# Performance work log

Hardware: AMD Instinct MI355X
Metric: run time of the kernel (lower is better)

## Reference

```python
import jax, jax.numpy as jnp
import numpy as np
from jax import lax

N_C = 1024  # number of FPS centroids (hard-coded in forward)
K = 32      # knn neighbors (hard-coded in forward)


def _fps(x, far0):
    # Faithful to the source: dist is recomputed against ONLY the latest
    # centroid each iteration (the mask/min-update in the source is dead code),
    # then far = argmax(dist).
    B = x.shape[0]
    bidx = jnp.arange(B)

    def step(far, _):
        c = x[bidx, far]                              # [B, C]
        d = jnp.sum((x - c[:, None, :]) ** 2, -1)     # [B, N]
        return jnp.argmax(d, -1), c

    _, cents = lax.scan(step, far0, None, length=N_C)  # cents: [n_c, B, C]
    return jnp.transpose(cents, (1, 0, 2))             # [B, n_c, C]


def _knn_group(x, cent):
    # squared euclidean distances (same argsort order as torch.cdist)
    d2 = (jnp.sum(cent ** 2, -1)[..., None]
          + jnp.sum(x ** 2, -1)[:, None, :]
          - 2.0 * jnp.einsum('bmc,bnc->bmn', cent, x))   # [B, n_c, N]
    _, idx = lax.top_k(-d2, K)                            # [B, n_c, K] smallest dists
    neighbors = jax.vmap(lambda xb, ib: xb[ib])(x, idx)   # [B, n_c, K, C]
    return neighbors


def _conv1x1(h, w, b):
    # 1x1 Conv1d == channel matmul; h: [B, Cin, L], w: [Cout, Cin]
    return jax.nn.relu(jnp.einsum('oi,bil->bol', w, h) + b[None, :, None])


def setup_inputs() -> dict:
    key = jax.random.key(0)
    ks = jax.random.split(key, 20)
    B, N, C = 4, 16384, 3
    num_classes = 3
    p = lambda k, shp: (jax.random.normal(k, shp, jnp.float32) * 0.02)
    return {
        'x': jax.random.normal(ks[0], (B, N, C), jnp.float32),
        'far_init': jax.random.randint(ks[1], (B,), 0, N, jnp.int32),
        'w1': p(ks[2], (64, 3)),    'b1': p(ks[3], (64,)),
        'w2': p(ks[4], (64, 64)),   'b2': p(ks[5], (64,)),
        'w3': p(ks[6], (64, 64)),   'b3': p(ks[7], (64,)),
        'w4': p(ks[8], (128, 64)),  'b4': p(ks[9], (128,)),
        'w5': p(ks[10], (1024, 128)), 'b5': p(ks[11], (1024,)),
        'fw1': p(ks[12], (512, 1024)), 'fb1': p(ks[13], (512,)),
        'fw2': p(ks[14], (256, 512)),  'fb2': p(ks[15], (256,)),
        'fw3': p(ks[16], (num_classes, 256)), 'fb3': p(ks[17], (num_classes,)),
    }


def reference(x, far_init, w1, b1, w2, b2, w3, b3, w4, b4, w5, b5,
              fw1, fb1, fw2, fb2, fw3, fb3):
    B, N, C = x.shape
    cent = _fps(x, far_init)                 # [B, n_c, C]
    neighbors = _knn_group(x, cent)          # [B, n_c, K, C]
    h = jnp.transpose(neighbors, (0, 3, 1, 2)).reshape(B, C, N_C * K)
    h = _conv1x1(h, w1, b1)
    h = _conv1x1(h, w2, b2)
    h = _conv1x1(h, w3, b3)
    h = _conv1x1(h, w4, b4)
    h = _conv1x1(h, w5, b5)                  # [B, 1024, n_c*K]
    g = jnp.max(h, axis=2)                   # global max pool -> [B, 1024]
    g = jax.nn.relu(g @ fw1.T + fb1)
    g = jax.nn.relu(g @ fw2.T + fb2)
    return g @ fw3.T + fb3                   # [B, num_classes]
```

## Files before the change

### kernel.cpp

```cpp
#include <hip/hip_runtime.h>

#define BN  4
#define NPT 16384
#define NCC 1024
#define KNN 32

#define HBINS    2048
#define CCH      2
#define CAND_CAP 768

#define NBLK 64

#define OFF_CCOUNT 0
#define OFF_SCOUNT 64
#define OFF_SBITS  128
#define OFF_POOL   (128 + BN*(NPT/32)*4)
#define OFF_CLIST  (OFF_POOL + BN*NCC*4)
#define OFF_H1     (OFF_CLIST + BN*NCC*4)
#define OFF_H2     (OFF_H1 + BN*512*4)
#define OFF_SLIST  (OFF_H2 + BN*256*4)
#define OFF_BAR    (OFF_SLIST + BN*NPT*4)

typedef short bf16x8 __attribute__((ext_vector_type(8)));
typedef float f32x4  __attribute__((ext_vector_type(4)));
typedef float f32x2  __attribute__((ext_vector_type(2)));

__device__ __forceinline__ short f2bf(float f) {
    unsigned u = __float_as_uint(f);
    return (short)((u + 0x7fffu + ((u >> 16) & 1u)) >> 16);
}
__device__ __forceinline__ bf16x8 cvt8(const float* __restrict__ p) {
    bf16x8 v;
#pragma unroll
    for (int j = 0; j < 8; ++j) v[j] = f2bf(p[j]);
    return v;
}

template <typename T>
__device__ __forceinline__ void ast(T* p, T v) {
    __hip_atomic_store(p, v, __ATOMIC_RELAXED, __HIP_MEMORY_SCOPE_AGENT);
}
template <typename T>
__device__ __forceinline__ T ald(const T* p) {
    return __hip_atomic_load(const_cast<T*>(p), __ATOMIC_RELAXED, __HIP_MEMORY_SCOPE_AGENT);
}

__device__ __forceinline__ void gridbar(unsigned* __restrict__ bar, int ph) {
    __syncthreads();
    if (threadIdx.x == 0) {
        __hip_atomic_fetch_add(&bar[ph], 1u, __ATOMIC_RELAXED, __HIP_MEMORY_SCOPE_AGENT);
        while (__hip_atomic_load(&bar[ph], __ATOMIC_RELAXED, __HIP_MEMORY_SCOPE_AGENT)
               < (unsigned)NBLK)
            __builtin_amdgcn_s_sleep(2);
    }
    __syncthreads();
}

__device__ __forceinline__ float pf4(const float* __restrict__ p, int nfloat,
                                     int t, float acc) {
    const float4* q = (const float4*)p;
    const int n4 = nfloat >> 2;
    for (int i = t; i < n4; i += 1024) {
        float4 v = q[i];
        acc += (v.x + v.y) + (v.z + v.w);
    }
    return acc;
}

__device__ __forceinline__ unsigned key_of(float px, float py, float pz, float xn,
                                           float cx, float cy, float cz, float cn)
{
    float dot = __fadd_rn(__fadd_rn(__fmul_rn(cx,px), __fmul_rn(cy,py)), __fmul_rn(cz,pz));
    float d2  = __fsub_rn(__fadd_rn(cn, xn), __fmul_rn(2.0f, dot));
    unsigned u = __float_as_uint(d2);
    return u ^ ((u >> 31) ? 0xFFFFFFFFu : 0x80000000u);
}

__device__ __forceinline__ void wave_scan_bins(const unsigned* __restrict__ H,
    int nbins, int rem, int lane, int* __restrict__ out_bin, int* __restrict__ out_below)
{
    int per = nbins >> 6;
    int base = lane * per;
    unsigned part = 0;
    for (int q = 0; q < per; ++q) part += H[base + q];
    unsigned inc = part;
#pragma unroll
    for (int m = 1; m < 64; m <<= 1) {
        unsigned u = __shfl_up(inc, m, 64);
        if (lane >= m) inc += u;
    }
    unsigned exc = inc - part;
    unsigned long long mk = __ballot(exc < (unsigned)rem && inc >= (unsigned)rem);
    int src = __ffsll((long long)mk) - 1;
    if (lane == src) {
        unsigned run = exc; int bb = base;
        for (int q = 0; q < per; ++q) {
            unsigned h = H[base + q];
            if (run + h >= (unsigned)rem) { bb = base + q; break; }
            run += h;
        }
        *out_bin = bb; *out_below = (int)run;
    }
}

#define MFMA16(a, bfr, c) __builtin_amdgcn_mfma_f32_16x16x32_bf16(a, bfr, c, 0, 0, 0)

__global__ __launch_bounds__(1024) void mega_kernel(const float* __restrict__ x,
    const int* __restrict__ far_init,
    const float* __restrict__ w1, const float* __restrict__ b1,
    const float* __restrict__ w2, const float* __restrict__ b2,
    const float* __restrict__ w3, const float* __restrict__ b3,
    const float* __restrict__ w4, const float* __restrict__ b4,
    const float* __restrict__ w5, const float* __restrict__ b5,
    const float* __restrict__ fw1, const float* __restrict__ fb1,
    const float* __restrict__ fw2, const float* __restrict__ fb2,
    const float* __restrict__ fw3, const float* __restrict__ fb3,
    int* __restrict__ clist, int* __restrict__ ccount, int* __restrict__ scount,
    unsigned* __restrict__ sbits, int* __restrict__ slist, float* __restrict__ pool,
    float* __restrict__ h1g, float* __restrict__ h2g, float* __restrict__ out,
    unsigned* __restrict__ bar)
{
    const int blk = blockIdx.x, t = threadIdx.x;
    __shared__ __align__(16) char smem[36864];

    {
#pragma clang fp contract(off)
        if (blk < 4) {
            const int b = blk;
            unsigned char* seen   = (unsigned char*)smem;
            unsigned*      vslot  = (unsigned*)(smem + 16384);
            int*           islot  = (int*)(smem + 16384 + 8);
            int*           nmatch = (int*)(smem + 16384 + 16);
            int4*          cslot  = (int4*)(smem + 16384 + 32);

            if (t < 512) ast(&sbits[b*(NPT/32) + t], 0u);
            ast(&pool[b*NCC + t], 0.0f);
            if (t == 0) { ast(&ccount[b], 0); ast(&scount[b], 0); }

            const float* xb = x + (size_t)b * NPT * 3;
            f32x2 px[8], py[8], pz[8];
#pragma unroll
            for (int r = 0; r < 8; ++r) {
                int ia = t + ((2*r) << 10), ib = ia + 1024;
                px[r] = f32x2{xb[ia*3+0], xb[ib*3+0]};
                py[r] = f32x2{xb[ia*3+1], xb[ib*3+1]};
                pz[r] = f32x2{xb[ia*3+2], xb[ib*3+2]};
            }
            ((uint4*)seen)[t] = make_uint4(0,0,0,0);
            if (t == 0) {
                vslot[0] = 0u;         vslot[1] = 0u;
                islot[0] = 0x7fffffff; islot[1] = 0x7fffffff;
                nmatch[0] = 0;         nmatch[1] = 0;
            }
            int prev_bx = far_init[b];
            __syncthreads();
            int pbs = __builtin_amdgcn_readfirstlane(prev_bx);
            float cx = xb[pbs*3], cy = xb[pbs*3+1], cz = xb[pbs*3+2];

            int done = 0;
            for (int it = 0; it < NCC-1; ++it) {
                const int p = it & 1;
                const f32x2 cX = {cx, cx}, cY = {cy, cy}, cZ = {cz, cz};
                f32x2 sv[8];
                f32x2 rm = {0.0f, 0.0f};
#pragma unroll
                for (int r = 0; r < 8; ++r) {
                    f32x2 dx = px[r] - cX;
                    f32x2 dy = py[r] - cY;
                    f32x2 dz = pz[r] - cZ;
                    f32x2 m1 = dx * dx;
                    f32x2 m2 = dy * dy;
                    f32x2 m3 = dz * dz;
                    f32x2 s  = (m1 + m2) + m3;
                    sv[r] = s;
                    rm.x = fmaxf(rm.x, s.x);
                    rm.y = fmaxf(rm.y, s.y);
                }
                float tm = fmaxf(rm.x, rm.y);
#pragma unroll
                for (int m = 1; m < 64; m <<= 1)
                    tm = fmaxf(tm, __shfl_xor(tm, m, 64));
                if ((t & 63) == 0) atomicMax(&vslot[p], __float_as_uint(tm));
                if (t == 0) seen[prev_bx] = 1;
                __syncthreads();
                const unsigned bmax = vslot[p];
                if (t == 0) {
                    vslot[p^1] = 0u; islot[p^1] = 0x7fffffff; nmatch[p^1] = 0;
                }
                if (__float_as_uint(tm) == bmax) {
                    int   myidx = 0x7fffffff;
                    float mx = 0.f, my = 0.f, mz = 0.f;
#pragma unroll
                    for (int r = 0; r < 8; ++r) {
                        int ia = t + ((2*r) << 10);
                        if (__float_as_uint(sv[r].x) == bmax && ia < myidx)
                            { myidx = ia;        mx = px[r].x; my = py[r].x; mz = pz[r].x; }
                        if (__float_as_uint(sv[r].y) == bmax && ia + 1024 < myidx)
                            { myidx = ia + 1024; mx = px[r].y; my = py[r].y; mz = pz[r].y; }
                    }
                    if (myidx != 0x7fffffff) {
                        atomicMin(&islot[p], myidx);
                        int cs = atomicAdd(&nmatch[p], 1);
                        if (cs < 4)
                            cslot[p*4 + cs] = make_int4(myidx, __float_as_int(mx),
                                                        __float_as_int(my), __float_as_int(mz));
                    }
                }
                __syncthreads();
                const int bx = islot[p];
                if (seen[bx]) { done = 1; break; }
                prev_bx = bx;
                const int nm = nmatch[p] < 4 ? nmatch[p] : 4;
                bool got = false;
                float nx = 0.f, ny = 0.f, nz = 0.f;
#pragma unroll
                for (int csi = 0; csi < 4; ++csi) {
                    if (csi < nm) {
                        int4 v = cslot[p*4 + csi];
                        if (v.x == bx) {
                            nx = __int_as_float(v.y); ny = __int_as_float(v.z);
                            nz = __int_as_float(v.w); got = true;
                        }
                    }
                }
                if (got) { cx = nx; cy = ny; cz = nz; }
                else {
                    int bxs = __builtin_amdgcn_readfirstlane(bx);
                    cx = xb[bxs*3]; cy = xb[bxs*3+1]; cz = xb[bxs*3+2];
                }
            }
            if (!done && t == 0) seen[prev_bx] = 1;
            __syncthreads();
#pragma unroll
            for (int j = 0; j < 16; ++j) {
                int idx = t + (j << 10);
                if (seen[idx]) {
                    int pos = atomicAdd(&ccount[b], 1);
                    ast(&clist[b * NCC + pos], idx);
                }
            }
        } else {
            float acc = 0.0f;
            const int bo = blk >> 2;
            acc = pf4(fw1 + bo*32*1024, 32*1024, t, acc);
            if (blk < 32) acc = pf4(fw2 + bo*32*512, 32*512, t, acc);
            acc = pf4(w5 + (bo & 3)*256*128, 256*128, t, acc);
            if (blk < 12) {
                acc = pf4(w2, 64*64, t, acc);
                acc = pf4(w3, 64*64, t, acc);
                acc = pf4(w4, 128*64, t, acc);
            }
            if (blk < 8) {
                acc = pf4(fw1, 32*1024, t, acc);
                acc = pf4(fw2, 32*512, t, acc);
            }
            asm volatile("" :: "v"(acc));
        }
    }
    gridbar(bar, 0);

    {
        const int c0 = ald(&ccount[0]), c1 = ald(&ccount[1]);
        const int c2 = ald(&ccount[2]), c3 = ald(&ccount[3]);
        const int maxc = max(max(c0,c1), max(c2,c3));
        unsigned* hist    = (unsigned*)smem;
        unsigned* cand    = (unsigned*)(smem + 16384);
        float*    cpx     = (float*)(smem + 22528);
        float*    cpy     = cpx + CCH;
        float*    cpz     = cpy + CCH;
        float*    cpn     = cpz + CCH;
        unsigned* candCnt = (unsigned*)(cpn + CCH);
        int*      s_bb    = (int*)(candCnt + CCH);
        int*      s_below = s_bb + CCH;
        int*      s_rrem  = s_below + CCH;
        int*      s_need  = s_rrem + CCH;
        int*      s_pref  = s_need + CCH;
        unsigned* s_tau   = (unsigned*)(s_pref + CCH);
        int*      s_tb    = (int*)(s_tau + CCH);

        const int lane = t & 63, w = t >> 6;

        for (int wi = blk; (wi >> 2) * CCH < maxc; wi += NBLK) {
            const int b = wi & 3;
            const int cnt = (b==0) ? c0 : (b==1) ? c1 : (b==2) ? c2 : c3;
            const int cbase = (wi >> 2) * CCH;
            if (cbase >= cnt) continue;
            const float* xb = x + (size_t)b * NPT * 3;

            __syncthreads();
            if (t < CCH) {
                int ci = ald(&clist[b * NCC + min(cbase + t, cnt - 1)]);
                float cx = xb[ci*3], cy = xb[ci*3+1], cz = xb[ci*3+2];
                cpx[t] = cx; cpy[t] = cy; cpz[t] = cz;
                cpn[t] = __fadd_rn(__fadd_rn(__fmul_rn(cx,cx), __fmul_rn(cy,cy)), __fmul_rn(cz,cz));
                candCnt[t] = 0;
            }
            for (int i = t; i < CCH * HBINS; i += 1024) hist[i] = 0;
            __syncthreads();

            unsigned keys[NPT/1024][CCH];
#pragma unroll
            for (int j = 0; j < NPT/1024; ++j) {
                int i = t + (j << 10);
                float px = xb[i*3], py = xb[i*3+1], pz = xb[i*3+2];
                float xn = __fadd_rn(__fadd_rn(__fmul_rn(px,px), __fmul_rn(py,py)), __fmul_rn(pz,pz));
#pragma unroll
                for (int c = 0; c < CCH; ++c) {
                    unsigned key = key_of(px,py,pz,xn, cpx[c],cpy[c],cpz[c],cpn[c]);
                    keys[j][c] = key;
                    atomicAdd(&hist[c*HBINS + (key >> 21)], 1u);
                }
            }
            __syncthreads();

            if (w < CCH)
                wave_scan_bins(&hist[w*HBINS], HBINS, KNN, lane, &s_bb[w], &s_below[w]);
            __syncthreads();
            if (t < CCH) s_rrem[t] = KNN - s_below[t];
            __syncthreads();

#pragma unroll
            for (int j = 0; j < NPT/1024; ++j) {
#pragma unroll
                for (int c = 0; c < CCH; ++c) {
                    unsigned key = keys[j][c];
                    if ((int)(key >> 21) == s_bb[c]) {
                        unsigned pos = atomicAdd(&candCnt[c], 1u);
                        if (pos < CAND_CAP) cand[c*CAND_CAP + pos] = key;
                    }
                }
            }
            __syncthreads();

            if (w < CCH) {
                unsigned cc = candCnt[w];
                if (cc <= CAND_CAP) {
                    int r = s_rrem[w] - 1;
                    const unsigned* C = &cand[w*CAND_CAP];
                    for (int idx = lane; idx < (int)cc; idx += 64) {
                        unsigned k = C[idx]; int rank = 0;
                        for (int q = 0; q < (int)cc; ++q) {
                            unsigned kq = C[q];
                            rank += (kq < k || (kq == k && q < idx)) ? 1 : 0;
                        }
                        if (rank == r) s_tau[w] = k;
                    }
                    if (lane == 0) s_need[w] = 0;
                } else if (lane == 0) s_need[w] = 1;
            }
            __syncthreads();

            for (int c = 0; c < CCH; ++c) {
                if (s_need[c]) {
                    const float cx = cpx[c], cy = cpy[c], cz = cpz[c], cn = cpn[c];
                    for (int i = t; i < HBINS; i += 1024) hist[i] = 0;
                    __syncthreads();
                    for (int j = 0; j < NPT/1024; ++j) {
                        int i = t + (j << 10);
                        float px = xb[i*3], py = xb[i*3+1], pz = xb[i*3+2];
                        float xn = __fadd_rn(__fadd_rn(__fmul_rn(px,px), __fmul_rn(py,py)), __fmul_rn(pz,pz));
                        unsigned key = key_of(px,py,pz,xn, cx,cy,cz,cn);
                        if ((int)(key >> 21) == s_bb[c]) atomicAdd(&hist[(key >> 10) & 2047u], 1u);
                    }
                    __syncthreads();
                    if (w == 0) wave_scan_bins(hist, HBINS, s_rrem[c], lane, &s_tb[0], &s_tb[1]);
                    __syncthreads();
                    if (t == 0) { s_pref[c] = (s_bb[c] << 11) | s_tb[0]; s_rrem[c] -= s_tb[1]; }
                    __syncthreads();
                    for (int i = t; i < 1024; i += 1024) hist[i] = 0;
                    __syncthreads();
                    for (int j = 0; j < NPT/1024; ++j) {
                        int i = t + (j << 10);
                        float px = xb[i*3], py = xb[i*3+1], pz = xb[i*3+2];
                        float xn = __fadd_rn(__fadd_rn(__fmul_rn(px,px), __fmul_rn(py,py)), __fmul_rn(pz,pz));
                        unsigned key = key_of(px,py,pz,xn, cx,cy,cz,cn);
                        if ((int)(key >> 10) == s_pref[c]) atomicAdd(&hist[key & 1023u], 1u);
                    }
                    __syncthreads();
                    if (w == 0) wave_scan_bins(hist, 1024, s_rrem[c], lane, &s_tb[0], &s_tb[1]);
                    __syncthreads();
                    if (t == 0) s_tau[c] = (((unsigned)s_pref[c]) << 10) | (unsigned)s_tb[0];
                    __syncthreads();
                }
            }
            __syncthreads();

#pragma unroll
            for (int j = 0; j < NPT/1024; ++j) {
                int i = t + (j << 10);
                bool sel = false;
#pragma unroll
                for (int c = 0; c < CCH; ++c) sel |= (keys[j][c] <= s_tau[c]);
                if (sel) {
                    unsigned bit = 1u << (i & 31);
                    unsigned old = atomicOr(&sbits[b*(NPT/32) + (i >> 5)], bit);
                    if (!(old & bit)) {
                        int pos = atomicAdd(&scount[b], 1);
                        ast(&slist[b * NPT + pos], i);
                    }
                }
            }
        }
    }
    gridbar(bar, 1);

    {
        const int s0 = ald(&scount[0]), s1 = ald(&scount[1]);
        const int s2 = ald(&scount[2]), s3 = ald(&scount[3]);
        short* A1 = (short*)smem;
        short* A2 = (short*)(smem + 9216);
        short* A3 = (short*)(smem + 18432);
        float* sx = (float*)(smem + 35840);

        const int lane = t & 63;
        const int w    = __builtin_amdgcn_readfirstlane(t >> 6);
        const int m    = lane & 15, quad = lane >> 4;
        const int b    = blk & 3;
        const int z    = (blk >> 2) & 3;
        const int cnt  = (b==0) ? s0 : (b==1) ? s1 : (b==2) ? s2 : s3;

        const int ocA = (w >> 2) * 16 + m;
        bf16x8 bw2[2], bw3[2], bw4[2][2], bw5[4];
#pragma unroll
        for (int ks = 0; ks < 2; ++ks) {
            bw2[ks] = cvt8(w2 + ocA*64 + ks*32 + quad*8);
            bw3[ks] = cvt8(w3 + ocA*64 + ks*32 + quad*8);
        }
        int oc4i[2];
#pragma unroll
        for (int r2 = 0; r2 < 2; ++r2) {
            oc4i[r2] = ((w >> 2) + 4*r2) * 16 + m;
#pragma unroll
            for (int ks = 0; ks < 2; ++ks)
                bw4[r2][ks] = cvt8(w4 + oc4i[r2]*64 + ks*32 + quad*8);
        }
        const int oc5 = z*256 + w*16 + m;
#pragma unroll
        for (int ks = 0; ks < 4; ++ks)
            bw5[ks] = cvt8(w5 + oc5*128 + ks*32 + quad*8);
        const float bias2 = b2[ocA], bias3 = b3[ocA];
        const float bias4_0 = b4[oc4i[0]], bias4_1 = b4[oc4i[1]];
        const float bias5 = b5[oc5];
        float w1v[4][3], b1v[4];
#pragma unroll
        for (int i = 0; i < 4; ++i) {
            int oc = w*4 + i;
            w1v[i][0] = w1[oc*3+0]; w1v[i][1] = w1[oc*3+1]; w1v[i][2] = w1[oc*3+2];
            b1v[i] = b1[oc];
        }
        const int pt0 = (w & 3) * 16;

        for (int xblk = blk >> 4; xblk * 64 < cnt; xblk += 4) {
            const int base = xblk << 6;
            const int npts = min(64, cnt - base);
            __syncthreads();
            if (t < 64) {
                int idx = ald(&slist[b * NPT + base + min(t, npts - 1)]);
                const float* xp = x + ((size_t)b * NPT + idx) * 3;
                sx[t] = xp[0]; sx[64 + t] = xp[1]; sx[128 + t] = xp[2];
            }
            __syncthreads();
            {
                float x0 = sx[lane], x1 = sx[64 + lane], x2 = sx[128 + lane];
#pragma unroll
                for (int i = 0; i < 4; ++i) {
                    float acc = fmaf(x2, w1v[i][2], fmaf(x1, w1v[i][1],
                                 fmaf(x0, w1v[i][0], b1v[i])));
                    A1[lane*72 + w*4 + i] = f2bf(fmaxf(acc, 0.0f));
                }
            }
            __syncthreads();
            {
                bf16x8 a0 = *(const bf16x8*)&A1[(pt0 + m)*72 + quad*8];
                bf16x8 a1 = *(const bf16x8*)&A1[(pt0 + m)*72 + 32 + quad*8];
                f32x4 d = {0.f, 0.f, 0.f, 0.f};
                d = MFMA16(a0, bw2[0], d);
                d = MFMA16(a1, bw2[1], d);
#pragma unroll
                for (int r = 0; r < 4; ++r)
                    A2[(pt0 + quad*4 + r)*72 + ocA] = f2bf(fmaxf(d[r] + bias2, 0.0f));
            }
            __syncthreads();
            {
                bf16x8 a0 = *(const bf16x8*)&A2[(pt0 + m)*72 + quad*8];
                bf16x8 a1 = *(const bf16x8*)&A2[(pt0 + m)*72 + 32 + quad*8];
                f32x4 d = {0.f, 0.f, 0.f, 0.f};
                d = MFMA16(a0, bw3[0], d);
                d = MFMA16(a1, bw3[1], d);
#pragma unroll
                for (int r = 0; r < 4; ++r)
                    A1[(pt0 + quad*4 + r)*72 + ocA] = f2bf(fmaxf(d[r] + bias3, 0.0f));
            }
            __syncthreads();
            {
                bf16x8 a0 = *(const bf16x8*)&A1[(pt0 + m)*72 + quad*8];
                bf16x8 a1 = *(const bf16x8*)&A1[(pt0 + m)*72 + 32 + quad*8];
#pragma unroll
                for (int r2 = 0; r2 < 2; ++r2) {
                    f32x4 d = {0.f, 0.f, 0.f, 0.f};
                    d = MFMA16(a0, bw4[r2][0], d);
                    d = MFMA16(a1, bw4[r2][1], d);
                    float bs = r2 ? bias4_1 : bias4_0;
#pragma unroll
                    for (int r = 0; r < 4; ++r)
                        A3[(pt0 + quad*4 + r)*136 + oc4i[r2]] = f2bf(fmaxf(d[r] + bs, 0.0f));
                }
            }
            __syncthreads();
            {
                float vm = 0.0f;
#pragma unroll
                for (int pt4 = 0; pt4 < 4; ++pt4) {
                    const int q0 = pt4 * 16;
                    f32x4 d = {0.f, 0.f, 0.f, 0.f};
#pragma unroll
                    for (int ks = 0; ks < 4; ++ks) {
                        bf16x8 a = *(const bf16x8*)&A3[(q0 + m)*136 + ks*32 + quad*8];
                        d = MFMA16(a, bw5[ks], d);
                    }
#pragma unroll
                    for (int r = 0; r < 4; ++r)
                        vm = fmaxf(vm, fmaxf(d[r] + bias5, 0.0f));
                }
                vm = fmaxf(vm, __shfl_xor(vm, 16, 64));
                vm = fmaxf(vm, __shfl_xor(vm, 32, 64));
                if (lane < 16)
                    atomicMax((int*)&pool[b*NCC + z*256 + w*16 + lane], __float_as_int(vm));
            }
        }
    }
    gridbar(bar, 2);

    {
        const int bo = blk >> 2, b = blk & 3;
        const int lane = t & 63, w = t >> 6;
        float* g = (float*)smem;
        g[t] = ald(&pool[b*NCC + t]);
        __syncthreads();
#pragma unroll
        for (int i = 0; i < 2; ++i) {
            int o = bo * 32 + w * 2 + i;
            float acc = 0.0f;
#pragma unroll
            for (int j = 0; j < 16; ++j) {
                int k = lane + (j << 6);
                acc += g[k] * fw1[o*1024 + k];
            }
#pragma unroll
            for (int m = 1; m < 64; m <<= 1) acc += __shfl_xor(acc, m, 64);
            if (lane == 0) ast(&h1g[b*512 + o], fmaxf(acc + fb1[o], 0.0f));
        }
    }
    gridbar(bar, 3);

    if (blk < 32) {
        const int bo = blk >> 2, b = blk & 3;
        const int lane = t & 63, w = t >> 6;
        float* h1 = (float*)smem;
        if (t < 512) h1[t] = ald(&h1g[b*512 + t]);
        __syncthreads();
#pragma unroll
        for (int i = 0; i < 2; ++i) {
            int o = bo * 32 + w * 2 + i;
            float acc = 0.0f;
#pragma unroll
            for (int j = 0; j < 8; ++j) {
                int k = lane + (j << 6);
                acc += h1[k] * fw2[o*512 + k];
            }
#pragma unroll
            for (int m = 1; m < 64; m <<= 1) acc += __shfl_xor(acc, m, 64);
            if (lane == 0) ast(&h2g[b*256 + o], fmaxf(acc + fb2[o], 0.0f));
        }
    }
    gridbar(bar, 4);

    if (blk < 4) {
        const int b = blk;
        const int lane = t & 63, w = t >> 6;
        float* h2 = (float*)smem;
        if (t < 256) h2[t] = ald(&h2g[b*256 + t]);
        __syncthreads();
        if (t < 256 && w < 3) {
            float acc = 0.0f;
#pragma unroll
            for (int j = 0; j < 4; ++j) {
                int k = lane + (j << 6);
                acc += h2[k] * fw3[w*256 + k];
            }
#pragma unroll
            for (int m = 1; m < 64; m <<= 1) acc += __shfl_xor(acc, m, 64);
            if (lane == 0) out[b*3 + w] = acc + fb3[w];
        }
    }
}

extern "C" void kernel_launch(void* const* d_in, const int* in_sizes, int n_in,
                              void* d_out, int out_size, void* d_ws, size_t ws_size,
                              hipStream_t stream)
{
    const float* x    = (const float*)d_in[0];
    const int*   far0 = (const int*)  d_in[1];
    const float *w1 = (const float*)d_in[2],  *b1 = (const float*)d_in[3];
    const float *w2 = (const float*)d_in[4],  *b2 = (const float*)d_in[5];
    const float *w3 = (const float*)d_in[6],  *b3 = (const float*)d_in[7];
    const float *w4 = (const float*)d_in[8],  *b4 = (const float*)d_in[9];
    const float *w5 = (const float*)d_in[10], *b5 = (const float*)d_in[11];
    const float *fw1 = (const float*)d_in[12], *fb1 = (const float*)d_in[13];
    const float *fw2 = (const float*)d_in[14], *fb2 = (const float*)d_in[15];
    const float *fw3 = (const float*)d_in[16], *fb3 = (const float*)d_in[17];

    char* ws = (char*)d_ws;
    int*      ccount = (int*)     (ws + OFF_CCOUNT);
    int*      scount = (int*)     (ws + OFF_SCOUNT);
    unsigned* sbits  = (unsigned*)(ws + OFF_SBITS);
    float*    pool   = (float*)   (ws + OFF_POOL);
    int*      clist  = (int*)     (ws + OFF_CLIST);
    float*    h1g    = (float*)   (ws + OFF_H1);
    float*    h2g    = (float*)   (ws + OFF_H2);
    int*      slist  = (int*)     (ws + OFF_SLIST);
    unsigned* bar    = (unsigned*)(ws + OFF_BAR);

    (void)hipMemsetAsync(bar, 0, 8 * sizeof(unsigned), stream);
    mega_kernel<<<NBLK, 1024, 0, stream>>>(x, far0,
        w1,b1, w2,b2, w3,b3, w4,b4, w5,b5, fw1,fb1, fw2,fb2, fw3,fb3,
        clist, ccount, scount, sbits, slist, pool, h1g, h2g, (float*)d_out, bar);
}
```

Before: 166.9 us.

## Split grid barriers into per-batch groups of 16 blocks

The 64 blocks are partitioned into four independent groups, one per batch, each with its own barrier counters, so a batch can move to KNN and the MLP stages as soon as its own FPS finishes instead of waiting for all four. Work distribution in each phase is remapped to local block indices within the group. The weight-prefetch warmup done by idle blocks during FPS is removed. The risk is losing that cache warming and uneven load if per-batch candidate counts differ, since groups can no longer rebalance work across batches.

```diff
diff --git a/kernel.cpp b/kernel.cpp
--- a/kernel.cpp
+++ b/kernel.cpp
@@ -10,6 +10,7 @@
 #define CAND_CAP 768
 
 #define NBLK 64
+#define GBLK 16
 
 #define OFF_CCOUNT 0
 #define OFF_SCOUNT 64
@@ -45,26 +46,14 @@
     return __hip_atomic_load(const_cast<T*>(p), __ATOMIC_RELAXED, __HIP_MEMORY_SCOPE_AGENT);
 }
 
-__device__ __forceinline__ void gridbar(unsigned* __restrict__ bar, int ph) {
+__device__ __forceinline__ void gridbar(unsigned* __restrict__ gbar, int ph, unsigned n) {
     __syncthreads();
     if (threadIdx.x == 0) {
-        __hip_atomic_fetch_add(&bar[ph], 1u, __ATOMIC_RELAXED, __HIP_MEMORY_SCOPE_AGENT);
-        while (__hip_atomic_load(&bar[ph], __ATOMIC_RELAXED, __HIP_MEMORY_SCOPE_AGENT)
-               < (unsigned)NBLK)
+        __hip_atomic_fetch_add(&gbar[ph], 1u, __ATOMIC_RELAXED, __HIP_MEMORY_SCOPE_AGENT);
+        while (__hip_atomic_load(&gbar[ph], __ATOMIC_RELAXED, __HIP_MEMORY_SCOPE_AGENT) < n)
             __builtin_amdgcn_s_sleep(2);
     }
     __syncthreads();
-}
-
-__device__ __forceinline__ float pf4(const float* __restrict__ p, int nfloat,
-                                     int t, float acc) {
-    const float4* q = (const float4*)p;
-    const int n4 = nfloat >> 2;
-    for (int i = t; i < n4; i += 1024) {
-        float4 v = q[i];
-        acc += (v.x + v.y) + (v.z + v.w);
-    }
-    return acc;
 }
 
 __device__ __forceinline__ unsigned key_of(float px, float py, float pz, float xn,
@@ -121,12 +110,15 @@
     unsigned* __restrict__ bar)
 {
     const int blk = blockIdx.x, t = threadIdx.x;
+    const int grp = blk >> 4;
+    const int lblk = blk & 15;
+    unsigned* gbar = bar + grp * 16;
     __shared__ __align__(16) char smem[36864];
 
     {
 #pragma clang fp contract(off)
-        if (blk < 4) {
-            const int b = blk;
+        if (lblk == 0) {
+            const int b = grp;
             unsigned char* seen   = (unsigned char*)smem;
             unsigned*      vslot  = (unsigned*)(smem + 16384);
             int*           islot  = (int*)(smem + 16384 + 8);
@@ -239,30 +231,13 @@
                     ast(&clist[b * NCC + pos], idx);
                 }
             }
-        } else {
-            float acc = 0.0f;
-            const int bo = blk >> 2;
-            acc = pf4(fw1 + bo*32*1024, 32*1024, t, acc);
-            if (blk < 32) acc = pf4(fw2 + bo*32*512, 32*512, t, acc);
-            acc = pf4(w5 + (bo & 3)*256*128, 256*128, t, acc);
-            if (blk < 12) {
-                acc = pf4(w2, 64*64, t, acc);
-                acc = pf4(w3, 64*64, t, acc);
-                acc = pf4(w4, 128*64, t, acc);
-            }
-            if (blk < 8) {
-                acc = pf4(fw1, 32*1024, t, acc);
-                acc = pf4(fw2, 32*512, t, acc);
-            }
-            asm volatile("" :: "v"(acc));
-        }
-    }
-    gridbar(bar, 0);
+        }
+    }
+    gridbar(gbar, 0, GBLK);
 
     {
-        const int c0 = ald(&ccount[0]), c1 = ald(&ccount[1]);
-        const int c2 = ald(&ccount[2]), c3 = ald(&ccount[3]);
-        const int maxc = max(max(c0,c1), max(c2,c3));
+        const int b = grp;
+        const int cnt = ald(&ccount[b]);
         unsigned* hist    = (unsigned*)smem;
         unsigned* cand    = (unsigned*)(smem + 16384);
         float*    cpx     = (float*)(smem + 22528);
@@ -279,13 +254,10 @@
         int*      s_tb    = (int*)(s_tau + CCH);
 
         const int lane = t & 63, w = t >> 6;
-
-        for (int wi = blk; (wi >> 2) * CCH < maxc; wi += NBLK) {
-            const int b = wi & 3;
-            const int cnt = (b==0) ? c0 : (b==1) ? c1 : (b==2) ? c2 : c3;
-            const int cbase = (wi >> 2) * CCH;
-            if (cbase >= cnt) continue;
-            const float* xb = x + (size_t)b * NPT * 3;
+        const float* xb = x + (size_t)b * NPT * 3;
+
+        for (int wi = lblk; wi * CCH < cnt; wi += GBLK) {
+            const int cbase = wi * CCH;
 
             __syncthreads();
             if (t < CCH) {
@@ -402,11 +374,11 @@
             }
         }
     }
-    gridbar(bar, 1);
+    gridbar(gbar, 1, GBLK);
 
     {
-        const int s0 = ald(&scount[0]), s1 = ald(&scount[1]);
-        const int s2 = ald(&scount[2]), s3 = ald(&scount[3]);
+        const int b = grp;
+        const int cnt = ald(&scount[b]);
         short* A1 = (short*)smem;
         short* A2 = (short*)(smem + 9216);
         short* A3 = (short*)(smem + 18432);
@@ -415,9 +387,7 @@
         const int lane = t & 63;
         const int w    = __builtin_amdgcn_readfirstlane(t >> 6);
         const int m    = lane & 15, quad = lane >> 4;
-        const int b    = blk & 3;
-        const int z    = (blk >> 2) & 3;
-        const int cnt  = (b==0) ? s0 : (b==1) ? s1 : (b==2) ? s2 : s3;
+        const int z    = lblk & 3;
 
         const int ocA = (w >> 2) * 16 + m;
         bf16x8 bw2[2], bw3[2], bw4[2][2], bw5[4];
@@ -450,7 +420,7 @@
         }
         const int pt0 = (w & 3) * 16;
 
-        for (int xblk = blk >> 4; xblk * 64 < cnt; xblk += 4) {
+        for (int xblk = lblk >> 2; xblk * 64 < cnt; xblk += 4) {
             const int base = xblk << 6;
             const int npts = min(64, cnt - base);
             __syncthreads();
@@ -529,10 +499,10 @@
             }
         }
     }
-    gridbar(bar, 2);
+    gridbar(gbar, 2, GBLK);
 
     {
-        const int bo = blk >> 2, b = blk & 3;
+        const int bo = lblk, b = grp;
         const int lane = t & 63, w = t >> 6;
         float* g = (float*)smem;
         g[t] = ald(&pool[b*NCC + t]);
@@ -551,10 +521,10 @@
             if (lane == 0) ast(&h1g[b*512 + o], fmaxf(acc + fb1[o], 0.0f));
         }
     }
-    gridbar(bar, 3);
-
-    if (blk < 32) {
-        const int bo = blk >> 2, b = blk & 3;
+    gridbar(gbar, 3, GBLK);
+
+    if (lblk < 8) {
+        const int bo = lblk, b = grp;
         const int lane = t & 63, w = t >> 6;
         float* h1 = (float*)smem;
         if (t < 512) h1[t] = ald(&h1g[b*512 + t]);
@@ -573,10 +543,10 @@
             if (lane == 0) ast(&h2g[b*256 + o], fmaxf(acc + fb2[o], 0.0f));
         }
     }
-    gridbar(bar, 4);
-
-    if (blk < 4) {
-        const int b = blk;
+    gridbar(gbar, 4, GBLK);
+
+    if (lblk == 0) {
+        const int b = grp;
         const int lane = t & 63, w = t >> 6;
         float* h2 = (float*)smem;
         if (t < 256) h2[t] = ald(&h2g[b*256 + t]);
@@ -621,7 +591,7 @@
     int*      slist  = (int*)     (ws + OFF_SLIST);
     unsigned* bar    = (unsigned*)(ws + OFF_BAR);
 
-    (void)hipMemsetAsync(bar, 0, 8 * sizeof(unsigned), stream);
+    (void)hipMemsetAsync(bar, 0, BN * 16 * sizeof(unsigned), stream);
     mega_kernel<<<NBLK, 1024, 0, stream>>>(x, far0,
         w1,b1, w2,b2, w3,b3, w4,b4, w5,b5, fw1,fb1, fw2,fb2, fw3,fb3,
         clist, ccount, scount, sbits, slist, pool, h1g, h2g, (float*)d_out, bar);
```

Measured after the change: 190.8 us. 14.3% more time.

## Use hierarchical grid barrier and drop idle-block weight prefetch

Applied to the files above, without the earlier changes.

Replaces the flat grid barrier, where every block spins on one counter, with a two-level scheme. Blocks arrive on 8 padded sub-counters, block 0 waits for all of them and then sets a go flag that the other blocks poll. It also removes the L2 warm-up loads of the MLP weights that idle blocks issued during FPS. The aim is less atomic contention at each barrier. The cost is an extra hop through block 0 and possibly colder weight loads in the later MLP stages.

```diff
diff --git a/kernel.cpp b/kernel.cpp
--- a/kernel.cpp
+++ b/kernel.cpp
@@ -47,24 +47,26 @@
 
 __device__ __forceinline__ void gridbar(unsigned* __restrict__ bar, int ph) {
     __syncthreads();
+    const int blk = blockIdx.x;
     if (threadIdx.x == 0) {
-        __hip_atomic_fetch_add(&bar[ph], 1u, __ATOMIC_RELAXED, __HIP_MEMORY_SCOPE_AGENT);
-        while (__hip_atomic_load(&bar[ph], __ATOMIC_RELAXED, __HIP_MEMORY_SCOPE_AGENT)
-               < (unsigned)NBLK)
-            __builtin_amdgcn_s_sleep(2);
+        unsigned* arr = bar + (ph*8 + (blk & 7)) * 16;
+        unsigned* go  = bar + (40 + ph) * 16;
+        __hip_atomic_fetch_add(arr, 1u, __ATOMIC_RELAXED, __HIP_MEMORY_SCOPE_AGENT);
+        if (blk == 0) {
+            for (int s = 0; s < 8; ++s) {
+                unsigned* a = bar + (ph*8 + s) * 16;
+                while (__hip_atomic_load(a, __ATOMIC_RELAXED,
+                                         __HIP_MEMORY_SCOPE_AGENT) < 8u)
+                    __builtin_amdgcn_s_sleep(1);
+            }
+            ast(go, 1u);
+        } else {
+            while (__hip_atomic_load(go, __ATOMIC_RELAXED,
+                                     __HIP_MEMORY_SCOPE_AGENT) == 0u)
+                __builtin_amdgcn_s_sleep(1);
+        }
     }
     __syncthreads();
-}
-
-__device__ __forceinline__ float pf4(const float* __restrict__ p, int nfloat,
-                                     int t, float acc) {
-    const float4* q = (const float4*)p;
-    const int n4 = nfloat >> 2;
-    for (int i = t; i < n4; i += 1024) {
-        float4 v = q[i];
-        acc += (v.x + v.y) + (v.z + v.w);
-    }
-    return acc;
 }
 
 __device__ __forceinline__ unsigned key_of(float px, float py, float pz, float xn,
@@ -239,22 +241,6 @@
                     ast(&clist[b * NCC + pos], idx);
                 }
             }
-        } else {
-            float acc = 0.0f;
-            const int bo = blk >> 2;
-            acc = pf4(fw1 + bo*32*1024, 32*1024, t, acc);
-            if (blk < 32) acc = pf4(fw2 + bo*32*512, 32*512, t, acc);
-            acc = pf4(w5 + (bo & 3)*256*128, 256*128, t, acc);
-            if (blk < 12) {
-                acc = pf4(w2, 64*64, t, acc);
-                acc = pf4(w3, 64*64, t, acc);
-                acc = pf4(w4, 128*64, t, acc);
-            }
-            if (blk < 8) {
-                acc = pf4(fw1, 32*1024, t, acc);
-                acc = pf4(fw2, 32*512, t, acc);
-            }
-            asm volatile("" :: "v"(acc));
         }
     }
     gridbar(bar, 0);
@@ -621,7 +607,7 @@
     int*      slist  = (int*)     (ws + OFF_SLIST);
     unsigned* bar    = (unsigned*)(ws + OFF_BAR);
 
-    (void)hipMemsetAsync(bar, 0, 8 * sizeof(unsigned), stream);
+    (void)hipMemsetAsync(bar, 0, 45 * 16 * sizeof(unsigned), stream);
     mega_kernel<<<NBLK, 1024, 0, stream>>>(x, far0,
         w1,b1, w2,b2, w3,b3, w4,b4, w5,b5, fw1,fb1, fw2,fb2, fw3,fb3,
         clist, ccount, scount, sbits, slist, pool, h1g, h2g, (float*)d_out, bar);
```

Result: no change. 169.5 us (+1.5%).

## Split grid barriers and preload FC weights into registers during barrier waits

Applied to the files above, without the earlier changes.

The grid barrier is split into separate arrive and wait steps. Between them, each block loads its slice of fw1 (and fw2) into registers, so those weight loads overlap the barrier wait instead of following it. The idle-block L2 prefetch sweep of fw1, fw2, w5, w2, w3 and w4 during the FPS phase is removed. This trades the earlier cache warming for a register-held prefetch placed just before the FC layers, which adds register pressure and may leave w5 and the conv weights cold in cache.

```diff
diff --git a/kernel.cpp b/kernel.cpp
--- a/kernel.cpp
+++ b/kernel.cpp
@@ -45,26 +45,22 @@
     return __hip_atomic_load(const_cast<T*>(p), __ATOMIC_RELAXED, __HIP_MEMORY_SCOPE_AGENT);
 }
 
-__device__ __forceinline__ void gridbar(unsigned* __restrict__ bar, int ph) {
+__device__ __forceinline__ void gb_arrive(unsigned* __restrict__ bar, int ph) {
     __syncthreads();
+    if (threadIdx.x == 0)
+        __hip_atomic_fetch_add(&bar[ph], 1u, __ATOMIC_RELAXED, __HIP_MEMORY_SCOPE_AGENT);
+}
+__device__ __forceinline__ void gb_wait(unsigned* __restrict__ bar, int ph) {
     if (threadIdx.x == 0) {
-        __hip_atomic_fetch_add(&bar[ph], 1u, __ATOMIC_RELAXED, __HIP_MEMORY_SCOPE_AGENT);
         while (__hip_atomic_load(&bar[ph], __ATOMIC_RELAXED, __HIP_MEMORY_SCOPE_AGENT)
                < (unsigned)NBLK)
             __builtin_amdgcn_s_sleep(2);
     }
     __syncthreads();
 }
-
-__device__ __forceinline__ float pf4(const float* __restrict__ p, int nfloat,
-                                     int t, float acc) {
-    const float4* q = (const float4*)p;
-    const int n4 = nfloat >> 2;
-    for (int i = t; i < n4; i += 1024) {
-        float4 v = q[i];
-        acc += (v.x + v.y) + (v.z + v.w);
-    }
-    return acc;
+__device__ __forceinline__ void gridbar(unsigned* __restrict__ bar, int ph) {
+    gb_arrive(bar, ph);
+    gb_wait(bar, ph);
 }
 
 __device__ __forceinline__ unsigned key_of(float px, float py, float pz, float xn,
@@ -239,22 +235,6 @@
                     ast(&clist[b * NCC + pos], idx);
                 }
             }
-        } else {
-            float acc = 0.0f;
-            const int bo = blk >> 2;
-            acc = pf4(fw1 + bo*32*1024, 32*1024, t, acc);
-            if (blk < 32) acc = pf4(fw2 + bo*32*512, 32*512, t, acc);
-            acc = pf4(w5 + (bo & 3)*256*128, 256*128, t, acc);
-            if (blk < 12) {
-                acc = pf4(w2, 64*64, t, acc);
-                acc = pf4(w3, 64*64, t, acc);
-                acc = pf4(w4, 128*64, t, acc);
-            }
-            if (blk < 8) {
-                acc = pf4(fw1, 32*1024, t, acc);
-                acc = pf4(fw2, 32*512, t, acc);
-            }
-            asm volatile("" :: "v"(acc));
         }
     }
     gridbar(bar, 0);
@@ -529,7 +509,20 @@
             }
         }
     }
-    gridbar(bar, 2);
+    gb_arrive(bar, 2);
+    float fw1r[32];
+    {
+        const int bo = blk >> 2;
+        const int lane = t & 63, w = t >> 6;
+#pragma unroll
+        for (int i = 0; i < 2; ++i) {
+            int o = bo * 32 + w * 2 + i;
+#pragma unroll
+            for (int j = 0; j < 16; ++j)
+                fw1r[i*16 + j] = fw1[o*1024 + lane + (j << 6)];
+        }
+    }
+    gb_wait(bar, 2);
 
     {
         const int bo = blk >> 2, b = blk & 3;
@@ -544,14 +537,27 @@
 #pragma unroll
             for (int j = 0; j < 16; ++j) {
                 int k = lane + (j << 6);
-                acc += g[k] * fw1[o*1024 + k];
+                acc += g[k] * fw1r[i*16 + j];
             }
 #pragma unroll
             for (int m = 1; m < 64; m <<= 1) acc += __shfl_xor(acc, m, 64);
             if (lane == 0) ast(&h1g[b*512 + o], fmaxf(acc + fb1[o], 0.0f));
         }
     }
-    gridbar(bar, 3);
+    gb_arrive(bar, 3);
+    float fw2r[16];
+    if (blk < 32) {
+        const int bo = blk >> 2;
+        const int lane = t & 63, w = t >> 6;
+#pragma unroll
+        for (int i = 0; i < 2; ++i) {
+            int o = bo * 32 + w * 2 + i;
+#pragma unroll
+            for (int j = 0; j < 8; ++j)
+                fw2r[i*8 + j] = fw2[o*512 + lane + (j << 6)];
+        }
+    }
+    gb_wait(bar, 3);
 
     if (blk < 32) {
         const int bo = blk >> 2, b = blk & 3;
@@ -566,7 +572,7 @@
 #pragma unroll
             for (int j = 0; j < 8; ++j) {
                 int k = lane + (j << 6);
-                acc += h1[k] * fw2[o*512 + k];
+                acc += h1[k] * fw2r[i*8 + j];
             }
 #pragma unroll
             for (int m = 1; m < 64; m <<= 1) acc += __shfl_xor(acc, m, 64);
```

New measurement: 164.0 us. About the same (-1.8%).
